# Kernel tuning notes

Hardware: AMD Instinct MI355X
Metric: run time of the kernel (lower is better)

## Reference

```python
import jax, jax.numpy as jnp
import numpy as np

B, S, H, NH, NKV, D = 1, 2048, 4096, 32, 8, 128
ROPE_BASE = 1000000.0


def setup_inputs() -> dict:
    key = jax.random.key(0)
    k0, k1, k2, k3, k4 = jax.random.split(key, 5)
    hidden_states = jax.random.normal(k0, (B, S, H), dtype=jnp.float32)
    Wq = jax.random.normal(k1, (NH * D, H), dtype=jnp.float32) * 0.02
    Wk = jax.random.normal(k2, (NKV * D, H), dtype=jnp.float32) * 0.02
    Wv = jax.random.normal(k3, (NKV * D, H), dtype=jnp.float32) * 0.02
    Wo = jax.random.normal(k4, (NH * D, NH * D), dtype=jnp.float32) * 0.02
    # RoPE tables (Mistral rope_theta = 1e6), concatenated-halves layout
    inv_freq = 1.0 / (ROPE_BASE ** (jnp.arange(0, D, 2, dtype=jnp.float32) / D))
    pos = jnp.arange(S, dtype=jnp.float32)
    freqs = pos[:, None] * inv_freq[None, :]            # [S, D/2]
    emb = jnp.concatenate([freqs, freqs], axis=-1)       # [S, D]
    cos = jnp.cos(emb)[None]                             # [1, S, D]
    sin = jnp.sin(emb)[None]
    # additive causal mask [1,1,S,S]
    causal = jnp.tril(jnp.ones((S, S), dtype=bool))
    attention_mask = jnp.where(causal, 0.0, -1e9).astype(jnp.float32)[None, None]
    return {"hidden_states": hidden_states, "cos": cos, "sin": sin,
            "attention_mask": attention_mask, "Wq": Wq, "Wk": Wk, "Wv": Wv, "Wo": Wo}


def _rotate_half(x):
    d = x.shape[-1] // 2
    return jnp.concatenate([-x[..., d:], x[..., :d]], axis=-1)


def reference(hidden_states, cos, sin, attention_mask, Wq, Wk, Wv, Wo):
    b, s, _ = hidden_states.shape
    nh = Wq.shape[0] // D
    nkv = Wk.shape[0] // D
    g = nh // nkv  # GQA groups
    scaling = D ** -0.5

    q = (hidden_states @ Wq.T).reshape(b, s, nh, D).transpose(0, 2, 1, 3)   # [b,nh,s,d]
    k = (hidden_states @ Wk.T).reshape(b, s, nkv, D).transpose(0, 2, 1, 3)  # [b,nkv,s,d]
    v = (hidden_states @ Wv.T).reshape(b, s, nkv, D).transpose(0, 2, 1, 3)

    c = cos[:, None]  # [b,1,s,d] broadcast over heads (unsqueeze_dim=1)
    sn = sin[:, None]
    q = q * c + _rotate_half(q) * sn
    k = k * c + _rotate_half(k) * sn

    # grouped-query attention without materializing repeated K/V
    qg = q.reshape(b, nkv, g, s, D)
    attn = jnp.einsum('bkgqd,bksd->bkgqs', qg, k) * scaling
    attn = attn + attention_mask[:, :, None]  # broadcast [1,1,1,s,s]
    w = jax.nn.softmax(attn.astype(jnp.float32), axis=-1).astype(q.dtype)
    out = jnp.einsum('bkgqs,bksd->bkgqd', w, v)  # [b,nkv,g,s,d]
    out = out.reshape(b, nh, s, D).transpose(0, 2, 1, 3).reshape(b, s, nh * D)
    return out @ Wo.T
```

## Files before the change

### kernel.cpp

```cpp
#include <hip/hip_runtime.h>
#include <hip/hip_bf16.h>
#include <cstdint>
#include <cstddef>

#define S_LEN 2048
#define HID   4096
#define NHEAD 32
#define NKVH  8
#define HD    128
#define QKV_STR 6144

typedef __bf16 bf16x8 __attribute__((ext_vector_type(8)));
typedef float  f32x4  __attribute__((ext_vector_type(4)));
typedef float  f32x16 __attribute__((ext_vector_type(16)));

__device__ __forceinline__ unsigned short f2bf(float f) {
  union { float f; unsigned int u; } c; c.f = f;
  unsigned int u = c.u;
  return (unsigned short)((u + 0x7fffu + ((u >> 16) & 1u)) >> 16);
}
__device__ __forceinline__ void gload16(const void* g, void* l) {
  __builtin_amdgcn_global_load_lds((const __attribute__((address_space(1))) void*)g,
                                   (__attribute__((address_space(3))) void*)l, 16, 0, 0);
}

__global__ void cvt_multi(const float* __restrict__ s0, const float* __restrict__ s1,
                          const float* __restrict__ s2, const float* __restrict__ s3,
                          const float* __restrict__ s4,
                          unsigned short* __restrict__ d0, unsigned short* __restrict__ d1,
                          unsigned short* __restrict__ d2, unsigned short* __restrict__ d3,
                          unsigned short* __restrict__ d4,
                          int n0, int n1, int n2, int n3, int n4c) {
  const float* src; unsigned short* dst; int n;
  switch (blockIdx.y) {
    case 0: src = s0; dst = d0; n = n0; break;
    case 1: src = s1; dst = d1; n = n1; break;
    case 2: src = s2; dst = d2; n = n2; break;
    case 3: src = s3; dst = d3; n = n3; break;
    default: src = s4; dst = d4; n = n4c; break;
  }
  int i = blockIdx.x * blockDim.x + threadIdx.x;
  int stride = gridDim.x * blockDim.x;
  for (; i < n; i += stride) {
    float4 v = ((const float4*)src)[i];
    ushort4 o;
    o.x = f2bf(v.x); o.y = f2bf(v.y); o.z = f2bf(v.z); o.w = f2bf(v.w);
    ((ushort4*)dst)[i] = o;
  }
}

template <bool F32OUT>
__global__ __launch_bounds__(256)
void gemm_bt(const unsigned short* __restrict__ A,
             const unsigned short* __restrict__ Bm,
             void* __restrict__ Cout, int N, int K) {
  __shared__ __align__(16) unsigned short lA[3][128 * 32];
  __shared__ __align__(16) unsigned short lB[3][128 * 32];
  const int tid = threadIdx.x;
  const int lane = tid & 63, wid = tid >> 6;
  const int l15 = lane & 15, lg = lane >> 4;
  const int wr = (wid >> 1) * 64, wc = (wid & 1) * 64;
  const int nwg = gridDim.x * 16;
  int bid = blockIdx.x + blockIdx.y * gridDim.x;
  bid = (bid & 7) * (nwg >> 3) + (bid >> 3);
  const int bm = bid & 15, bn = bid >> 4;

  f32x4 acc[4][4] = {};
  const unsigned short* Ab = A + (size_t)bm * 128 * K;
  const unsigned short* Bb = Bm + (size_t)bn * 128 * K;

  auto stage = [&](int t, int buf) {
    const int k0 = t * 32;
#pragma unroll
    for (int i = 0; i < 2; ++i) {
      int c = tid + i * 256;
      int row = c >> 2, sl = c & 3;
      int g = sl ^ ((row >> 1) & 3);
      gload16(Ab + (size_t)row * K + k0 + g * 8, (char*)lA[buf] + c * 16);
      gload16(Bb + (size_t)row * K + k0 + g * 8, (char*)lB[buf] + c * 16);
    }
  };

  const int nt = K / 32;
  stage(0, 0);
  if (nt > 1) stage(1, 1);
  const int swz = (l15 >> 1) & 3;

  int cur = 0;
  for (int t = 0; t < nt; ++t) {
    if (t + 1 < nt) asm volatile("s_waitcnt vmcnt(4)" ::: "memory");
    else            asm volatile("s_waitcnt vmcnt(0)" ::: "memory");
    __builtin_amdgcn_s_barrier();
    __builtin_amdgcn_sched_barrier(0);
    if (t + 2 < nt) { int nb = cur + 2; if (nb >= 3) nb -= 3; stage(t + 2, nb); }
    bf16x8 af[4], bfr[4];
#pragma unroll
    for (int m = 0; m < 4; ++m)
      af[m] = *(const bf16x8*)&lA[cur][(wr + m * 16 + l15) * 32 + ((lg ^ swz) * 8)];
#pragma unroll
    for (int n = 0; n < 4; ++n)
      bfr[n] = *(const bf16x8*)&lB[cur][(wc + n * 16 + l15) * 32 + ((lg ^ swz) * 8)];
#pragma unroll
    for (int m = 0; m < 4; ++m)
#pragma unroll
      for (int n = 0; n < 4; ++n)
        acc[m][n] = __builtin_amdgcn_mfma_f32_16x16x32_bf16(af[m], bfr[n], acc[m][n], 0, 0, 0);
    ++cur; if (cur >= 3) cur -= 3;
  }
  const int r0 = bm * 128 + wr + 4 * lg;
  const int c0 = bn * 128 + wc + l15;
#pragma unroll
  for (int m = 0; m < 4; ++m)
#pragma unroll
    for (int n = 0; n < 4; ++n)
#pragma unroll
      for (int j = 0; j < 4; ++j) {
        size_t idx = (size_t)(r0 + m * 16 + j) * N + (c0 + n * 16);
        if (F32OUT) ((float*)Cout)[idx] = acc[m][n][j];
        else        ((unsigned short*)Cout)[idx] = f2bf(acc[m][n][j]);
      }
}

__global__ void rope_kernel(unsigned short* __restrict__ X,
                            const float* __restrict__ cp,
                            const float* __restrict__ sp, int lognh, int rs) {
  int idx = blockIdx.x * blockDim.x + threadIdx.x;
  int d = idx & 63;
  int head = (idx >> 6) & ((1 << lognh) - 1);
  int s = idx >> (6 + lognh);
  float c = cp[s * 128 + d], sn = sp[s * 128 + d];
  size_t base = (size_t)s * rs + (head << 7) + d;
  float x1 = __bfloat162float(*(const __hip_bfloat16*)&X[base]);
  float x2 = __bfloat162float(*(const __hip_bfloat16*)&X[base + 64]);
  X[base]      = f2bf(x1 * c - x2 * sn);
  X[base + 64] = f2bf(x2 * c + x1 * sn);
}

__global__ __launch_bounds__(256)
void transpose_v(const unsigned short* __restrict__ qkv,
                 unsigned short* __restrict__ VT) {
  __shared__ __align__(16) unsigned short tile[128 * 128];
  const int tid = threadIdx.x;
  const int s0 = blockIdx.x * 128;
  const int kvh = blockIdx.y;
  const unsigned short* src = qkv + 5120 + kvh * 128;
#pragma unroll
  for (int i = 0; i < 8; ++i) {
    int c = tid + i * 256;
    int s = c >> 4, dc = c & 15;
    int f = (s ^ (s >> 3)) & 7;
    uint4 v = *(const uint4*)(src + (size_t)(s0 + s) * QKV_STR + dc * 8);
    *(uint4*)&tile[s * 128 + ((dc ^ f) * 8)] = v;
  }
  __syncthreads();
#pragma unroll
  for (int i = 0; i < 8; ++i) {
    int c = tid + i * 256;
    int d = c >> 4, sc = c & 15;
    unsigned short tmp[8];
#pragma unroll
    for (int j = 0; j < 8; ++j) {
      int s = sc * 8 + j;
      int f = (s ^ (s >> 3)) & 7;
      tmp[j] = tile[s * 128 + (((d >> 3) ^ f) * 8) + (d & 7)];
    }
    *(uint4*)(VT + ((size_t)kvh * 128 + d) * S_LEN + s0 + sc * 8) = *(uint4*)tmp;
  }
}

#define CROW(r) (((r) & 3) + 8 * ((r) >> 2) + 4 * hi)
__global__ __launch_bounds__(256, 2)
void flash_attn(const unsigned short* __restrict__ qkv,
                const unsigned short* __restrict__ VT,
                unsigned short* __restrict__ Og) {
  __shared__ __align__(16) unsigned short lK[2 * 64 * 128];
  __shared__ __align__(16) unsigned short lVt[2 * 128 * 64];
  const int tid = threadIdx.x;
  const int lane = tid & 63, w = tid >> 6;
  const int l31 = lane & 31, hi = lane >> 5;
  const int h = blockIdx.y, kvh = h >> 2;
  const int qt = (gridDim.x - 1) - blockIdx.x;
  const int nt = 2 * qt + 2;
  const int qlane = qt * 128 + w * 32 + l31;
  const int qmaxw = qt * 128 + w * 32 + 31;
  const float S2 = 0.12752960f;

  bf16x8 qf[8];
  {
    const unsigned short* qp = qkv + (size_t)qlane * QKV_STR + h * HD + hi * 8;
#pragma unroll
    for (int ks = 0; ks < 8; ++ks) qf[ks] = *(const bf16x8*)(qp + ks * 16);
  }
  f32x16 accO[4] = {};
  float m_run = -3e38f, l_run = 0.f;

  const unsigned short* Kb0 = qkv + 4096 + kvh * HD;
  const unsigned short* VTh = VT + (size_t)kvh * 128 * S_LEN;

  auto stageK = [&](int t, int buf) {
    const unsigned short* Kb = Kb0 + (size_t)(t * 64) * QKV_STR;
    char* dst = (char*)(lK + buf * (64 * 128));
#pragma unroll
    for (int i = 0; i < 4; ++i) {
      int c = tid + i * 256;
      int row = c >> 4, s = c & 15;
      gload16(Kb + (size_t)row * QKV_STR + ((s ^ (row & 7)) * 8), dst + c * 16);
    }
  };
  auto stageV = [&](int t, int buf) {
    const unsigned short* Vb = VTh + t * 64;
    char* dst = (char*)(lVt + buf * (128 * 64));
#pragma unroll
    for (int i = 0; i < 4; ++i) {
      int c = tid + i * 256;
      int d = c >> 3, s = c & 7;
      gload16(Vb + (size_t)d * S_LEN + ((s ^ (d & 7)) * 8), dst + c * 16);
    }
  };

  stageK(0, 0);
  stageV(0, 0);
  __syncthreads();

  int cur = 0;
  for (int t = 0; t < nt; ++t) {
    const bool pf = (t + 1 < nt);
    if (pf) { stageK(t + 1, cur ^ 1); stageV(t + 1, cur ^ 1); }

#pragma unroll
    for (int c2 = 0; c2 < 2; ++c2) {
      const int kvb = t * 64 + c2 * 32;
      if (kvb > qmaxw) continue;
      f32x16 st = {};
      const unsigned short* lKc = lK + cur * (64 * 128) + c2 * 32 * 128;
      __builtin_amdgcn_s_setprio(1);
#pragma unroll
      for (int ks = 0; ks < 8; ++ks) {
        bf16x8 kf = *(const bf16x8*)&lKc[l31 * 128 + (((ks * 2 + hi) ^ (l31 & 7)) * 8)];
        st = __builtin_amdgcn_mfma_f32_32x32x16_bf16(kf, qf[ks], st, 0, 0, 0);
      }
      __builtin_amdgcn_s_setprio(0);
      if (kvb + 31 > qt * 128 + w * 32) {
#pragma unroll
        for (int r = 0; r < 16; ++r)
          if (kvb + CROW(r) > qlane) st[r] = -3e38f;
      }
      float t0 = fmaxf(st[0], st[1]),  t1 = fmaxf(st[2], st[3]);
      float t2 = fmaxf(st[4], st[5]),  t3 = fmaxf(st[6], st[7]);
      float t4 = fmaxf(st[8], st[9]),  t5 = fmaxf(st[10], st[11]);
      float t6 = fmaxf(st[12], st[13]), t7 = fmaxf(st[14], st[15]);
      float tm = fmaxf(fmaxf(fmaxf(t0, t1), fmaxf(t2, t3)),
                       fmaxf(fmaxf(t4, t5), fmaxf(t6, t7)));
      tm = fmaxf(tm, __shfl_xor(tm, 32));
      const bool skip = __all(tm <= m_run);
      float corr = 1.f;
      if (!skip) {
        float mnew = fmaxf(m_run, tm);
        corr = __builtin_amdgcn_exp2f((m_run - mnew) * S2);
        m_run = mnew;
      }
      const float mS2 = m_run * S2;
      float p[16];
#pragma unroll
      for (int r = 0; r < 16; ++r) p[r] = __builtin_amdgcn_exp2f(st[r] * S2 - mS2);
      float s0b = (p[0] + p[1]) + (p[2] + p[3]);
      float s1b = (p[4] + p[5]) + (p[6] + p[7]);
      float s2b = (p[8] + p[9]) + (p[10] + p[11]);
      float s3b = (p[12] + p[13]) + (p[14] + p[15]);
      float rsum = (s0b + s1b) + (s2b + s3b);
      rsum += __shfl_xor(rsum, 32);
      l_run = l_run * corr + rsum;
      if (!skip) {
#pragma unroll
        for (int db = 0; db < 4; ++db) accO[db] = accO[db] * corr;
      }
      unsigned wpk[8], xpk[8];
#pragma unroll
      for (int i = 0; i < 8; ++i) {
        __hip_bfloat162 b2 = __float22bfloat162_rn(float2{p[2 * i], p[2 * i + 1]});
        wpk[i] = *(unsigned*)&b2;
        xpk[i] = (unsigned)__shfl_xor((int)wpk[i], 32);
      }
      int4 pa0i, pa1i;
      pa0i.x = hi ? (int)xpk[2] : (int)wpk[0]; pa0i.y = hi ? (int)xpk[3] : (int)wpk[1];
      pa0i.z = hi ? (int)wpk[2] : (int)xpk[0]; pa0i.w = hi ? (int)wpk[3] : (int)xpk[1];
      pa1i.x = hi ? (int)xpk[6] : (int)wpk[4]; pa1i.y = hi ? (int)xpk[7] : (int)wpk[5];
      pa1i.z = hi ? (int)wpk[6] : (int)xpk[4]; pa1i.w = hi ? (int)wpk[7] : (int)xpk[5];
      bf16x8 pa0 = *(bf16x8*)&pa0i, pa1 = *(bf16x8*)&pa1i;
      const unsigned short* lVc = lVt + cur * (128 * 64);
      __builtin_amdgcn_s_setprio(1);
#pragma unroll
      for (int db = 0; db < 4; ++db) {
        int d = db * 32 + l31;
#pragma unroll
        for (int ks2 = 0; ks2 < 2; ++ks2) {
          int ck = c2 * 4 + ks2 * 2 + hi;
          bf16x8 vf = *(const bf16x8*)&lVc[d * 64 + ((ck ^ (d & 7)) * 8)];
          accO[db] = __builtin_amdgcn_mfma_f32_32x32x16_bf16(vf, ks2 ? pa1 : pa0, accO[db], 0, 0, 0);
        }
      }
      __builtin_amdgcn_s_setprio(0);
    }
    __syncthreads();
    cur ^= 1;
  }

  const float invl = 1.0f / l_run;
  unsigned short* orow = Og + (size_t)(qt * 128 + w * 32 + l31) * HID + h * HD;
#pragma unroll
  for (int db = 0; db < 4; ++db)
#pragma unroll
    for (int rr = 0; rr < 4; ++rr) {
      int d0 = db * 32 + rr * 8 + 4 * hi;
      ushort4 o;
      o.x = f2bf(accO[db][rr * 4 + 0] * invl);
      o.y = f2bf(accO[db][rr * 4 + 1] * invl);
      o.z = f2bf(accO[db][rr * 4 + 2] * invl);
      o.w = f2bf(accO[db][rr * 4 + 3] * invl);
      *(ushort4*)(orow + d0) = o;
    }
}

extern "C" void kernel_launch(void* const* d_in, const int* in_sizes, int n_in,
                              void* d_out, int out_size, void* d_ws, size_t ws_size,
                              hipStream_t stream) {
  const float* hs   = (const float*)d_in[0];
  const float* cosp = (const float*)d_in[1];
  const float* sinp = (const float*)d_in[2];
  const float* Wq = (const float*)d_in[4];
  const float* Wk = (const float*)d_in[5];
  const float* Wv = (const float*)d_in[6];
  const float* Wo = (const float*)d_in[7];
  float* out = (float*)d_out;

  uint8_t* ws = (uint8_t*)d_ws;
  size_t off = 0;
  auto alloc = [&](size_t bytes) { void* p = ws + off; off += bytes; return p; };
  unsigned short* hidB  = (unsigned short*)alloc((size_t)S_LEN * HID * 2);
  unsigned short* wqkvB = (unsigned short*)alloc((size_t)QKV_STR * HID * 2);
  unsigned short* woB   = (unsigned short*)alloc((size_t)HID * HID * 2);
  unsigned short* qkvB  = (unsigned short*)alloc((size_t)S_LEN * QKV_STR * 2);
  unsigned short* aoB   = (unsigned short*)alloc((size_t)S_LEN * HID * 2);
  unsigned short* vtB   = (unsigned short*)alloc((size_t)NKVH * HD * S_LEN * 2);

  cvt_multi<<<dim3(1024, 5), 256, 0, stream>>>(
      hs, Wq, Wk, Wv, Wo,
      hidB, wqkvB, wqkvB + (size_t)HID * HID, wqkvB + (size_t)(HID + 1024) * HID, woB,
      S_LEN * HID / 4, HID * HID / 4, 1024 * HID / 4, 1024 * HID / 4, HID * HID / 4);

  gemm_bt<false><<<dim3(QKV_STR / 128, S_LEN / 128), 256, 0, stream>>>(
      hidB, wqkvB, qkvB, QKV_STR, HID);

  rope_kernel<<<(S_LEN * NHEAD * 64) / 256, 256, 0, stream>>>(qkvB, cosp, sinp, 5, QKV_STR);
  rope_kernel<<<(S_LEN * NKVH * 64) / 256, 256, 0, stream>>>(qkvB + HID, cosp, sinp, 3, QKV_STR);

  transpose_v<<<dim3(S_LEN / 128, NKVH), 256, 0, stream>>>(qkvB, vtB);

  flash_attn<<<dim3(S_LEN / 128, NHEAD), 256, 0, stream>>>(qkvB, vtB, aoB);

  gemm_bt<true><<<dim3(HID / 128, S_LEN / 128), 256, 0, stream>>>(
      aoB, woB, out, HID, HID);
}
```

Measured before the change: 367.4 us.

## Templatize GEMM tile shape, add lazy softmax rescale and permlane32 swap

```diff
diff --git a/kernel.cpp b/kernel.cpp
--- a/kernel.cpp
+++ b/kernel.cpp
@@ -13,6 +13,7 @@
 typedef __bf16 bf16x8 __attribute__((ext_vector_type(8)));
 typedef float  f32x4  __attribute__((ext_vector_type(4)));
 typedef float  f32x16 __attribute__((ext_vector_type(16)));
+typedef unsigned uint32x2_t __attribute__((ext_vector_type(2)));
 
 __device__ __forceinline__ unsigned short f2bf(float f) {
   union { float f; unsigned int u; } c; c.f = f;
@@ -49,34 +50,42 @@
   }
 }
 
-template <bool F32OUT>
-__global__ __launch_bounds__(256)
+template <int MR, int NR, bool F32OUT>
+__global__ __launch_bounds__(256, 2)
 void gemm_bt(const unsigned short* __restrict__ A,
              const unsigned short* __restrict__ Bm,
              void* __restrict__ Cout, int N, int K) {
-  __shared__ __align__(16) unsigned short lA[3][128 * 32];
-  __shared__ __align__(16) unsigned short lB[3][128 * 32];
+  constexpr int BM = 32 * MR, BN = 32 * NR;
+  constexpr int BLKM = 2048 / BM;
+  __shared__ __align__(16) unsigned short lA[3][BM * 32];
+  __shared__ __align__(16) unsigned short lB[3][BN * 32];
   const int tid = threadIdx.x;
   const int lane = tid & 63, wid = tid >> 6;
   const int l15 = lane & 15, lg = lane >> 4;
-  const int wr = (wid >> 1) * 64, wc = (wid & 1) * 64;
-  const int nwg = gridDim.x * 16;
+  const int wr = (wid >> 1) * (BM / 2), wc = (wid & 1) * (BN / 2);
+  const int nwg = gridDim.x * gridDim.y;
   int bid = blockIdx.x + blockIdx.y * gridDim.x;
   bid = (bid & 7) * (nwg >> 3) + (bid >> 3);
-  const int bm = bid & 15, bn = bid >> 4;
-
-  f32x4 acc[4][4] = {};
-  const unsigned short* Ab = A + (size_t)bm * 128 * K;
-  const unsigned short* Bb = Bm + (size_t)bn * 128 * K;
+  const int bm = bid % BLKM, bn = bid / BLKM;
+
+  f32x4 acc[MR][NR] = {};
+  const unsigned short* Ab = A + (size_t)bm * BM * K;
+  const unsigned short* Bb = Bm + (size_t)bn * BN * K;
 
   auto stage = [&](int t, int buf) {
     const int k0 = t * 32;
 #pragma unroll
-    for (int i = 0; i < 2; ++i) {
+    for (int i = 0; i < BM / 64; ++i) {
       int c = tid + i * 256;
       int row = c >> 2, sl = c & 3;
       int g = sl ^ ((row >> 1) & 3);
       gload16(Ab + (size_t)row * K + k0 + g * 8, (char*)lA[buf] + c * 16);
+    }
+#pragma unroll
+    for (int i = 0; i < BN / 64; ++i) {
+      int c = tid + i * 256;
+      int row = c >> 2, sl = c & 3;
+      int g = sl ^ ((row >> 1) & 3);
       gload16(Bb + (size_t)row * K + k0 + g * 8, (char*)lB[buf] + c * 16);
     }
   };
@@ -88,31 +97,35 @@
 
   int cur = 0;
   for (int t = 0; t < nt; ++t) {
-    if (t + 1 < nt) asm volatile("s_waitcnt vmcnt(4)" ::: "memory");
-    else            asm volatile("s_waitcnt vmcnt(0)" ::: "memory");
+    if (t + 1 < nt) {
+      if constexpr ((BM + BN) / 64 == 4) asm volatile("s_waitcnt vmcnt(4)" ::: "memory");
+      else                               asm volatile("s_waitcnt vmcnt(6)" ::: "memory");
+    } else {
+      asm volatile("s_waitcnt vmcnt(0)" ::: "memory");
+    }
     __builtin_amdgcn_s_barrier();
     __builtin_amdgcn_sched_barrier(0);
     if (t + 2 < nt) { int nb = cur + 2; if (nb >= 3) nb -= 3; stage(t + 2, nb); }
-    bf16x8 af[4], bfr[4];
-#pragma unroll
-    for (int m = 0; m < 4; ++m)
+    bf16x8 af[MR], bfr[NR];
+#pragma unroll
+    for (int m = 0; m < MR; ++m)
       af[m] = *(const bf16x8*)&lA[cur][(wr + m * 16 + l15) * 32 + ((lg ^ swz) * 8)];
 #pragma unroll
-    for (int n = 0; n < 4; ++n)
+    for (int n = 0; n < NR; ++n)
       bfr[n] = *(const bf16x8*)&lB[cur][(wc + n * 16 + l15) * 32 + ((lg ^ swz) * 8)];
 #pragma unroll
-    for (int m = 0; m < 4; ++m)
-#pragma unroll
-      for (int n = 0; n < 4; ++n)
+    for (int m = 0; m < MR; ++m)
+#pragma unroll
+      for (int n = 0; n < NR; ++n)
         acc[m][n] = __builtin_amdgcn_mfma_f32_16x16x32_bf16(af[m], bfr[n], acc[m][n], 0, 0, 0);
     ++cur; if (cur >= 3) cur -= 3;
   }
-  const int r0 = bm * 128 + wr + 4 * lg;
-  const int c0 = bn * 128 + wc + l15;
-#pragma unroll
-  for (int m = 0; m < 4; ++m)
-#pragma unroll
-    for (int n = 0; n < 4; ++n)
+  const int r0 = bm * BM + wr + 4 * lg;
+  const int c0 = bn * BN + wc + l15;
+#pragma unroll
+  for (int m = 0; m < MR; ++m)
+#pragma unroll
+    for (int n = 0; n < NR; ++n)
 #pragma unroll
       for (int j = 0; j < 4; ++j) {
         size_t idx = (size_t)(r0 + m * 16 + j) * N + (c0 + n * 16);
@@ -252,7 +265,7 @@
       float tm = fmaxf(fmaxf(fmaxf(t0, t1), fmaxf(t2, t3)),
                        fmaxf(fmaxf(t4, t5), fmaxf(t6, t7)));
       tm = fmaxf(tm, __shfl_xor(tm, 32));
-      const bool skip = __all(tm <= m_run);
+      const bool skip = __all((tm - m_run) * S2 <= 8.0f);
       float corr = 1.f;
       if (!skip) {
         float mnew = fmaxf(m_run, tm);
@@ -274,18 +287,29 @@
 #pragma unroll
         for (int db = 0; db < 4; ++db) accO[db] = accO[db] * corr;
       }
-      unsigned wpk[8], xpk[8];
+      unsigned wpk[8];
 #pragma unroll
       for (int i = 0; i < 8; ++i) {
         __hip_bfloat162 b2 = __float22bfloat162_rn(float2{p[2 * i], p[2 * i + 1]});
         wpk[i] = *(unsigned*)&b2;
-        xpk[i] = (unsigned)__shfl_xor((int)wpk[i], 32);
       }
       int4 pa0i, pa1i;
+#if __has_builtin(__builtin_amdgcn_permlane32_swap)
+      uint32x2_t r0 = __builtin_amdgcn_permlane32_swap(wpk[0], wpk[2], false, false);
+      uint32x2_t r1 = __builtin_amdgcn_permlane32_swap(wpk[1], wpk[3], false, false);
+      uint32x2_t r2 = __builtin_amdgcn_permlane32_swap(wpk[4], wpk[6], false, false);
+      uint32x2_t r3 = __builtin_amdgcn_permlane32_swap(wpk[5], wpk[7], false, false);
+      pa0i.x = (int)r0.x; pa0i.y = (int)r1.x; pa0i.z = (int)r0.y; pa0i.w = (int)r1.y;
+      pa1i.x = (int)r2.x; pa1i.y = (int)r3.x; pa1i.z = (int)r2.y; pa1i.w = (int)r3.y;
+#else
+      unsigned xpk[8];
+#pragma unroll
+      for (int i = 0; i < 8; ++i) xpk[i] = (unsigned)__shfl_xor((int)wpk[i], 32);
       pa0i.x = hi ? (int)xpk[2] : (int)wpk[0]; pa0i.y = hi ? (int)xpk[3] : (int)wpk[1];
       pa0i.z = hi ? (int)wpk[2] : (int)xpk[0]; pa0i.w = hi ? (int)wpk[3] : (int)xpk[1];
       pa1i.x = hi ? (int)xpk[6] : (int)wpk[4]; pa1i.y = hi ? (int)xpk[7] : (int)wpk[5];
       pa1i.z = hi ? (int)wpk[6] : (int)xpk[4]; pa1i.w = hi ? (int)wpk[7] : (int)xpk[5];
+#endif
       bf16x8 pa0 = *(bf16x8*)&pa0i, pa1 = *(bf16x8*)&pa1i;
       const unsigned short* lVc = lVt + cur * (128 * 64);
       __builtin_amdgcn_s_setprio(1);
@@ -348,7 +372,7 @@
       hidB, wqkvB, wqkvB + (size_t)HID * HID, wqkvB + (size_t)(HID + 1024) * HID, woB,
       S_LEN * HID / 4, HID * HID / 4, 1024 * HID / 4, 1024 * HID / 4, HID * HID / 4);
 
-  gemm_bt<false><<<dim3(QKV_STR / 128, S_LEN / 128), 256, 0, stream>>>(
+  gemm_bt<8, 4, false><<<dim3(QKV_STR / 128, S_LEN / 256), 256, 0, stream>>>(
       hidB, wqkvB, qkvB, QKV_STR, HID);
 
   rope_kernel<<<(S_LEN * NHEAD * 64) / 256, 256, 0, stream>>>(qkvB, cosp, sinp, 5, QKV_STR);
@@ -358,6 +382,6 @@
 
   flash_attn<<<dim3(S_LEN / 128, NHEAD), 256, 0, stream>>>(qkvB, vtB, aoB);
 
-  gemm_bt<true><<<dim3(HID / 128, S_LEN / 128), 256, 0, stream>>>(
+  gemm_bt<4, 4, true><<<dim3(HID / 128, S_LEN / 128), 256, 0, stream>>>(
       aoB, woB, out, HID, HID);
 }
```

Result: slower. 376.8 us (+2.5%).

## Use 8-wave 128x256 GEMM tiles, lazy softmax rescale, and permlane32 swap

Applied to the files above, without the earlier changes.

```diff
diff --git a/kernel.cpp b/kernel.cpp
--- a/kernel.cpp
+++ b/kernel.cpp
@@ -13,6 +13,7 @@
 typedef __bf16 bf16x8 __attribute__((ext_vector_type(8)));
 typedef float  f32x4  __attribute__((ext_vector_type(4)));
 typedef float  f32x16 __attribute__((ext_vector_type(16)));
+typedef unsigned uint32x2_t __attribute__((ext_vector_type(2)));
 
 __device__ __forceinline__ unsigned short f2bf(float f) {
   union { float f; unsigned int u; } c; c.f = f;
@@ -50,65 +51,136 @@
 }
 
 template <bool F32OUT>
-__global__ __launch_bounds__(256)
-void gemm_bt(const unsigned short* __restrict__ A,
-             const unsigned short* __restrict__ Bm,
-             void* __restrict__ Cout, int N, int K) {
-  __shared__ __align__(16) unsigned short lA[3][128 * 32];
-  __shared__ __align__(16) unsigned short lB[3][128 * 32];
+__global__ __launch_bounds__(512, 1)
+void gemm8p(const unsigned short* __restrict__ A,
+            const unsigned short* __restrict__ Bm,
+            void* __restrict__ Cout, int N, int K) {
+  __shared__ __align__(16) unsigned short lA[3][128 * 64];
+  __shared__ __align__(16) unsigned short lB[3][256 * 64];
   const int tid = threadIdx.x;
   const int lane = tid & 63, wid = tid >> 6;
   const int l15 = lane & 15, lg = lane >> 4;
-  const int wr = (wid >> 1) * 64, wc = (wid & 1) * 64;
-  const int nwg = gridDim.x * 16;
+  const int wm = wid >> 2, wn = wid & 3;
+  const int wr = wm * 64, wc = wn * 64;
+  const int nwg = gridDim.x * gridDim.y;
   int bid = blockIdx.x + blockIdx.y * gridDim.x;
   bid = (bid & 7) * (nwg >> 3) + (bid >> 3);
   const int bm = bid & 15, bn = bid >> 4;
 
   f32x4 acc[4][4] = {};
   const unsigned short* Ab = A + (size_t)bm * 128 * K;
-  const unsigned short* Bb = Bm + (size_t)bn * 128 * K;
-
-  auto stage = [&](int t, int buf) {
-    const int k0 = t * 32;
+  const unsigned short* Bb = Bm + (size_t)bn * 256 * K;
+
+  auto stageA = [&](int t, int buf) {
+    const int k0 = t * 64;
 #pragma unroll
     for (int i = 0; i < 2; ++i) {
-      int c = tid + i * 256;
-      int row = c >> 2, sl = c & 3;
-      int g = sl ^ ((row >> 1) & 3);
+      int c = tid + i * 512;
+      int row = c >> 3, ch = c & 7;
+      int g = ch ^ (row & 7);
       gload16(Ab + (size_t)row * K + k0 + g * 8, (char*)lA[buf] + c * 16);
+    }
+  };
+  auto stageB = [&](int t, int buf, int half) {
+    const int k0 = t * 64;
+#pragma unroll
+    for (int i = 0; i < 2; ++i) {
+      int c = tid + (half * 2 + i) * 512;
+      int row = c >> 3, ch = c & 7;
+      int g = ch ^ (row & 7);
       gload16(Bb + (size_t)row * K + k0 + g * 8, (char*)lB[buf] + c * 16);
     }
   };
-
-  const int nt = K / 32;
-  stage(0, 0);
-  if (nt > 1) stage(1, 1);
-  const int swz = (l15 >> 1) & 3;
+  auto rdA = [&](int buf, int m, int ks) -> bf16x8 {
+    int row = wr + m * 16 + l15;
+    int ch = (ks * 4 + lg) ^ (row & 7);
+    return *(const bf16x8*)&lA[buf][row * 64 + ch * 8];
+  };
+  auto rdB = [&](int buf, int n, int ks) -> bf16x8 {
+    int row = wc + n * 16 + l15;
+    int ch = (ks * 4 + lg) ^ (row & 7);
+    return *(const bf16x8*)&lB[buf][row * 64 + ch * 8];
+  };
+
+  const int nt = K / 64;
+  stageA(0, 0); stageB(0, 0, 0); stageB(0, 0, 1);
+  stageA(1, 1); stageB(1, 1, 0); stageB(1, 1, 1);
 
   int cur = 0;
   for (int t = 0; t < nt; ++t) {
-    if (t + 1 < nt) asm volatile("s_waitcnt vmcnt(4)" ::: "memory");
+    if (t + 1 < nt) asm volatile("s_waitcnt vmcnt(6)" ::: "memory");
     else            asm volatile("s_waitcnt vmcnt(0)" ::: "memory");
     __builtin_amdgcn_s_barrier();
     __builtin_amdgcn_sched_barrier(0);
-    if (t + 2 < nt) { int nb = cur + 2; if (nb >= 3) nb -= 3; stage(t + 2, nb); }
-    bf16x8 af[4], bfr[4];
-#pragma unroll
-    for (int m = 0; m < 4; ++m)
-      af[m] = *(const bf16x8*)&lA[cur][(wr + m * 16 + l15) * 32 + ((lg ^ swz) * 8)];
-#pragma unroll
-    for (int n = 0; n < 4; ++n)
-      bfr[n] = *(const bf16x8*)&lB[cur][(wc + n * 16 + l15) * 32 + ((lg ^ swz) * 8)];
-#pragma unroll
-    for (int m = 0; m < 4; ++m)
-#pragma unroll
-      for (int n = 0; n < 4; ++n)
-        acc[m][n] = __builtin_amdgcn_mfma_f32_16x16x32_bf16(af[m], bfr[n], acc[m][n], 0, 0, 0);
+    int nb = cur + 2; if (nb >= 3) nb -= 3;
+    const bool pf = (t + 2 < nt);
+    bf16x8 b0, b1, b2, b3, a0, a1;
+
+    if (pf) stageA(t + 2, nb);
+    a0 = rdA(cur, 0, 0); a1 = rdA(cur, 1, 0);
+    b0 = rdB(cur, 0, 0); b1 = rdB(cur, 1, 0);
+    b2 = rdB(cur, 2, 0); b3 = rdB(cur, 3, 0);
+    __builtin_amdgcn_s_setprio(1);
+    acc[0][0] = __builtin_amdgcn_mfma_f32_16x16x32_bf16(a0, b0, acc[0][0], 0, 0, 0);
+    acc[0][1] = __builtin_amdgcn_mfma_f32_16x16x32_bf16(a0, b1, acc[0][1], 0, 0, 0);
+    acc[0][2] = __builtin_amdgcn_mfma_f32_16x16x32_bf16(a0, b2, acc[0][2], 0, 0, 0);
+    acc[0][3] = __builtin_amdgcn_mfma_f32_16x16x32_bf16(a0, b3, acc[0][3], 0, 0, 0);
+    acc[1][0] = __builtin_amdgcn_mfma_f32_16x16x32_bf16(a1, b0, acc[1][0], 0, 0, 0);
+    acc[1][1] = __builtin_amdgcn_mfma_f32_16x16x32_bf16(a1, b1, acc[1][1], 0, 0, 0);
+    acc[1][2] = __builtin_amdgcn_mfma_f32_16x16x32_bf16(a1, b2, acc[1][2], 0, 0, 0);
+    acc[1][3] = __builtin_amdgcn_mfma_f32_16x16x32_bf16(a1, b3, acc[1][3], 0, 0, 0);
+    __builtin_amdgcn_s_setprio(0);
+    __builtin_amdgcn_s_barrier();
+    __builtin_amdgcn_sched_barrier(0);
+
+    if (pf) stageB(t + 2, nb, 0);
+    a0 = rdA(cur, 2, 0); a1 = rdA(cur, 3, 0);
+    __builtin_amdgcn_s_setprio(1);
+    acc[2][0] = __builtin_amdgcn_mfma_f32_16x16x32_bf16(a0, b0, acc[2][0], 0, 0, 0);
+    acc[2][1] = __builtin_amdgcn_mfma_f32_16x16x32_bf16(a0, b1, acc[2][1], 0, 0, 0);
+    acc[2][2] = __builtin_amdgcn_mfma_f32_16x16x32_bf16(a0, b2, acc[2][2], 0, 0, 0);
+    acc[2][3] = __builtin_amdgcn_mfma_f32_16x16x32_bf16(a0, b3, acc[2][3], 0, 0, 0);
+    acc[3][0] = __builtin_amdgcn_mfma_f32_16x16x32_bf16(a1, b0, acc[3][0], 0, 0, 0);
+    acc[3][1] = __builtin_amdgcn_mfma_f32_16x16x32_bf16(a1, b1, acc[3][1], 0, 0, 0);
+    acc[3][2] = __builtin_amdgcn_mfma_f32_16x16x32_bf16(a1, b2, acc[3][2], 0, 0, 0);
+    acc[3][3] = __builtin_amdgcn_mfma_f32_16x16x32_bf16(a1, b3, acc[3][3], 0, 0, 0);
+    __builtin_amdgcn_s_setprio(0);
+    __builtin_amdgcn_s_barrier();
+    __builtin_amdgcn_sched_barrier(0);
+
+    if (pf) stageB(t + 2, nb, 1);
+    a0 = rdA(cur, 0, 1); a1 = rdA(cur, 1, 1);
+    b0 = rdB(cur, 0, 1); b1 = rdB(cur, 1, 1);
+    b2 = rdB(cur, 2, 1); b3 = rdB(cur, 3, 1);
+    __builtin_amdgcn_s_setprio(1);
+    acc[0][0] = __builtin_amdgcn_mfma_f32_16x16x32_bf16(a0, b0, acc[0][0], 0, 0, 0);
+    acc[0][1] = __builtin_amdgcn_mfma_f32_16x16x32_bf16(a0, b1, acc[0][1], 0, 0, 0);
+    acc[0][2] = __builtin_amdgcn_mfma_f32_16x16x32_bf16(a0, b2, acc[0][2], 0, 0, 0);
+    acc[0][3] = __builtin_amdgcn_mfma_f32_16x16x32_bf16(a0, b3, acc[0][3], 0, 0, 0);
+    acc[1][0] = __builtin_amdgcn_mfma_f32_16x16x32_bf16(a1, b0, acc[1][0], 0, 0, 0);
+    acc[1][1] = __builtin_amdgcn_mfma_f32_16x16x32_bf16(a1, b1, acc[1][1], 0, 0, 0);
+    acc[1][2] = __builtin_amdgcn_mfma_f32_16x16x32_bf16(a1, b2, acc[1][2], 0, 0, 0);
+    acc[1][3] = __builtin_amdgcn_mfma_f32_16x16x32_bf16(a1, b3, acc[1][3], 0, 0, 0);
+    __builtin_amdgcn_s_setprio(0);
+    __builtin_amdgcn_s_barrier();
+    __builtin_amdgcn_sched_barrier(0);
+
+    a0 = rdA(cur, 2, 1); a1 = rdA(cur, 3, 1);
+    __builtin_amdgcn_s_setprio(1);
+    acc[2][0] = __builtin_amdgcn_mfma_f32_16x16x32_bf16(a0, b0, acc[2][0], 0, 0, 0);
+    acc[2][1] = __builtin_amdgcn_mfma_f32_16x16x32_bf16(a0, b1, acc[2][1], 0, 0, 0);
+    acc[2][2] = __builtin_amdgcn_mfma_f32_16x16x32_bf16(a0, b2, acc[2][2], 0, 0, 0);
+    acc[2][3] = __builtin_amdgcn_mfma_f32_16x16x32_bf16(a0, b3, acc[2][3], 0, 0, 0);
+    acc[3][0] = __builtin_amdgcn_mfma_f32_16x16x32_bf16(a1, b0, acc[3][0], 0, 0, 0);
+    acc[3][1] = __builtin_amdgcn_mfma_f32_16x16x32_bf16(a1, b1, acc[3][1], 0, 0, 0);
+    acc[3][2] = __builtin_amdgcn_mfma_f32_16x16x32_bf16(a1, b2, acc[3][2], 0, 0, 0);
+    acc[3][3] = __builtin_amdgcn_mfma_f32_16x16x32_bf16(a1, b3, acc[3][3], 0, 0, 0);
+    __builtin_amdgcn_s_setprio(0);
     ++cur; if (cur >= 3) cur -= 3;
   }
+
   const int r0 = bm * 128 + wr + 4 * lg;
-  const int c0 = bn * 128 + wc + l15;
+  const int c0 = bn * 256 + wc + l15;
 #pragma unroll
   for (int m = 0; m < 4; ++m)
 #pragma unroll
@@ -252,7 +324,7 @@
       float tm = fmaxf(fmaxf(fmaxf(t0, t1), fmaxf(t2, t3)),
                        fmaxf(fmaxf(t4, t5), fmaxf(t6, t7)));
       tm = fmaxf(tm, __shfl_xor(tm, 32));
-      const bool skip = __all(tm <= m_run);
+      const bool skip = __all((tm - m_run) * S2 <= 8.0f);
       float corr = 1.f;
       if (!skip) {
         float mnew = fmaxf(m_run, tm);
@@ -274,18 +346,29 @@
 #pragma unroll
         for (int db = 0; db < 4; ++db) accO[db] = accO[db] * corr;
       }
-      unsigned wpk[8], xpk[8];
+      unsigned wpk[8];
 #pragma unroll
       for (int i = 0; i < 8; ++i) {
         __hip_bfloat162 b2 = __float22bfloat162_rn(float2{p[2 * i], p[2 * i + 1]});
         wpk[i] = *(unsigned*)&b2;
-        xpk[i] = (unsigned)__shfl_xor((int)wpk[i], 32);
       }
       int4 pa0i, pa1i;
+#if __has_builtin(__builtin_amdgcn_permlane32_swap)
+      uint32x2_t r0 = __builtin_amdgcn_permlane32_swap(wpk[0], wpk[2], false, false);
+      uint32x2_t r1 = __builtin_amdgcn_permlane32_swap(wpk[1], wpk[3], false, false);
+      uint32x2_t r2 = __builtin_amdgcn_permlane32_swap(wpk[4], wpk[6], false, false);
+      uint32x2_t r3 = __builtin_amdgcn_permlane32_swap(wpk[5], wpk[7], false, false);
+      pa0i.x = (int)r0.x; pa0i.y = (int)r1.x; pa0i.z = (int)r0.y; pa0i.w = (int)r1.y;
+      pa1i.x = (int)r2.x; pa1i.y = (int)r3.x; pa1i.z = (int)r2.y; pa1i.w = (int)r3.y;
+#else
+      unsigned xpk[8];
+#pragma unroll
+      for (int i = 0; i < 8; ++i) xpk[i] = (unsigned)__shfl_xor((int)wpk[i], 32);
       pa0i.x = hi ? (int)xpk[2] : (int)wpk[0]; pa0i.y = hi ? (int)xpk[3] : (int)wpk[1];
       pa0i.z = hi ? (int)wpk[2] : (int)xpk[0]; pa0i.w = hi ? (int)wpk[3] : (int)xpk[1];
       pa1i.x = hi ? (int)xpk[6] : (int)wpk[4]; pa1i.y = hi ? (int)xpk[7] : (int)wpk[5];
       pa1i.z = hi ? (int)wpk[6] : (int)xpk[4]; pa1i.w = hi ? (int)wpk[7] : (int)xpk[5];
+#endif
       bf16x8 pa0 = *(bf16x8*)&pa0i, pa1 = *(bf16x8*)&pa1i;
       const unsigned short* lVc = lVt + cur * (128 * 64);
       __builtin_amdgcn_s_setprio(1);
@@ -348,7 +431,7 @@
       hidB, wqkvB, wqkvB + (size_t)HID * HID, wqkvB + (size_t)(HID + 1024) * HID, woB,
       S_LEN * HID / 4, HID * HID / 4, 1024 * HID / 4, 1024 * HID / 4, HID * HID / 4);
 
-  gemm_bt<false><<<dim3(QKV_STR / 128, S_LEN / 128), 256, 0, stream>>>(
+  gemm8p<false><<<dim3(QKV_STR / 256, S_LEN / 128), 512, 0, stream>>>(
       hidB, wqkvB, qkvB, QKV_STR, HID);
 
   rope_kernel<<<(S_LEN * NHEAD * 64) / 256, 256, 0, stream>>>(qkvB, cosp, sinp, 5, QKV_STR);
@@ -358,6 +441,6 @@
 
   flash_attn<<<dim3(S_LEN / 128, NHEAD), 256, 0, stream>>>(qkvB, vtB, aoB);
 
-  gemm_bt<true><<<dim3(HID / 128, S_LEN / 128), 256, 0, stream>>>(
+  gemm8p<true><<<dim3(HID / 256, S_LEN / 128), 512, 0, stream>>>(
       aoB, woB, out, HID, HID);
 }
```

New measurement: 484.2 us. 31.8% more time.

## Fuse Q RoPE into attention, lazy max rescale, permlane32 swap for P

Applied to the files above, without the earlier changes.

```diff
diff --git a/kernel.cpp b/kernel.cpp
--- a/kernel.cpp
+++ b/kernel.cpp
@@ -13,11 +13,16 @@
 typedef __bf16 bf16x8 __attribute__((ext_vector_type(8)));
 typedef float  f32x4  __attribute__((ext_vector_type(4)));
 typedef float  f32x16 __attribute__((ext_vector_type(16)));
+typedef unsigned uint32x2_t __attribute__((ext_vector_type(2)));
 
 __device__ __forceinline__ unsigned short f2bf(float f) {
   union { float f; unsigned int u; } c; c.f = f;
   unsigned int u = c.u;
   return (unsigned short)((u + 0x7fffu + ((u >> 16) & 1u)) >> 16);
+}
+__device__ __forceinline__ float bf2f(unsigned short b) {
+  union { unsigned int u; float f; } c; c.u = ((unsigned int)b) << 16;
+  return c.f;
 }
 __device__ __forceinline__ void gload16(const void* g, void* l) {
   __builtin_amdgcn_global_load_lds((const __attribute__((address_space(1))) void*)g,
@@ -130,8 +135,8 @@
   int s = idx >> (6 + lognh);
   float c = cp[s * 128 + d], sn = sp[s * 128 + d];
   size_t base = (size_t)s * rs + (head << 7) + d;
-  float x1 = __bfloat162float(*(const __hip_bfloat16*)&X[base]);
-  float x2 = __bfloat162float(*(const __hip_bfloat16*)&X[base + 64]);
+  float x1 = bf2f(X[base]);
+  float x2 = bf2f(X[base + 64]);
   X[base]      = f2bf(x1 * c - x2 * sn);
   X[base + 64] = f2bf(x2 * c + x1 * sn);
 }
@@ -172,6 +177,8 @@
 __global__ __launch_bounds__(256, 2)
 void flash_attn(const unsigned short* __restrict__ qkv,
                 const unsigned short* __restrict__ VT,
+                const float* __restrict__ cp,
+                const float* __restrict__ sp,
                 unsigned short* __restrict__ Og) {
   __shared__ __align__(16) unsigned short lK[2 * 64 * 128];
   __shared__ __align__(16) unsigned short lVt[2 * 128 * 64];
@@ -190,6 +197,23 @@
     const unsigned short* qp = qkv + (size_t)qlane * QKV_STR + h * HD + hi * 8;
 #pragma unroll
     for (int ks = 0; ks < 8; ++ks) qf[ks] = *(const bf16x8*)(qp + ks * 16);
+    const float* crow = cp + (size_t)qlane * 128 + hi * 8;
+    const float* srow = sp + (size_t)qlane * 128 + hi * 8;
+#pragma unroll
+    for (int ks = 0; ks < 4; ++ks) {
+      float4 c0 = *(const float4*)(crow + ks * 16);
+      float4 c1 = *(const float4*)(crow + ks * 16 + 4);
+      float4 s0 = *(const float4*)(srow + ks * 16);
+      float4 s1 = *(const float4*)(srow + ks * 16 + 4);
+      float cc[8] = {c0.x, c0.y, c0.z, c0.w, c1.x, c1.y, c1.z, c1.w};
+      float ss[8] = {s0.x, s0.y, s0.z, s0.w, s1.x, s1.y, s1.z, s1.w};
+#pragma unroll
+      for (int j = 0; j < 8; ++j) {
+        float x1 = (float)qf[ks][j], x2 = (float)qf[ks + 4][j];
+        qf[ks][j]     = (__bf16)(x1 * cc[j] - x2 * ss[j]);
+        qf[ks + 4][j] = (__bf16)(x2 * cc[j] + x1 * ss[j]);
+      }
+    }
   }
   f32x16 accO[4] = {};
   float m_run = -3e38f, l_run = 0.f;
@@ -252,7 +276,7 @@
       float tm = fmaxf(fmaxf(fmaxf(t0, t1), fmaxf(t2, t3)),
                        fmaxf(fmaxf(t4, t5), fmaxf(t6, t7)));
       tm = fmaxf(tm, __shfl_xor(tm, 32));
-      const bool skip = __all(tm <= m_run);
+      const bool skip = __all((tm - m_run) * S2 <= 8.0f);
       float corr = 1.f;
       if (!skip) {
         float mnew = fmaxf(m_run, tm);
@@ -274,18 +298,29 @@
 #pragma unroll
         for (int db = 0; db < 4; ++db) accO[db] = accO[db] * corr;
       }
-      unsigned wpk[8], xpk[8];
+      unsigned wpk[8];
 #pragma unroll
       for (int i = 0; i < 8; ++i) {
         __hip_bfloat162 b2 = __float22bfloat162_rn(float2{p[2 * i], p[2 * i + 1]});
         wpk[i] = *(unsigned*)&b2;
-        xpk[i] = (unsigned)__shfl_xor((int)wpk[i], 32);
       }
       int4 pa0i, pa1i;
+#if __has_builtin(__builtin_amdgcn_permlane32_swap)
+      uint32x2_t r0 = __builtin_amdgcn_permlane32_swap(wpk[0], wpk[2], false, false);
+      uint32x2_t r1 = __builtin_amdgcn_permlane32_swap(wpk[1], wpk[3], false, false);
+      uint32x2_t r2 = __builtin_amdgcn_permlane32_swap(wpk[4], wpk[6], false, false);
+      uint32x2_t r3 = __builtin_amdgcn_permlane32_swap(wpk[5], wpk[7], false, false);
+      pa0i.x = (int)r0.x; pa0i.y = (int)r1.x; pa0i.z = (int)r0.y; pa0i.w = (int)r1.y;
+      pa1i.x = (int)r2.x; pa1i.y = (int)r3.x; pa1i.z = (int)r2.y; pa1i.w = (int)r3.y;
+#else
+      unsigned xpk[8];
+#pragma unroll
+      for (int i = 0; i < 8; ++i) xpk[i] = (unsigned)__shfl_xor((int)wpk[i], 32);
       pa0i.x = hi ? (int)xpk[2] : (int)wpk[0]; pa0i.y = hi ? (int)xpk[3] : (int)wpk[1];
       pa0i.z = hi ? (int)wpk[2] : (int)xpk[0]; pa0i.w = hi ? (int)wpk[3] : (int)xpk[1];
       pa1i.x = hi ? (int)xpk[6] : (int)wpk[4]; pa1i.y = hi ? (int)xpk[7] : (int)wpk[5];
       pa1i.z = hi ? (int)wpk[6] : (int)xpk[4]; pa1i.w = hi ? (int)wpk[7] : (int)xpk[5];
+#endif
       bf16x8 pa0 = *(bf16x8*)&pa0i, pa1 = *(bf16x8*)&pa1i;
       const unsigned short* lVc = lVt + cur * (128 * 64);
       __builtin_amdgcn_s_setprio(1);
@@ -351,12 +386,11 @@
   gemm_bt<false><<<dim3(QKV_STR / 128, S_LEN / 128), 256, 0, stream>>>(
       hidB, wqkvB, qkvB, QKV_STR, HID);
 
-  rope_kernel<<<(S_LEN * NHEAD * 64) / 256, 256, 0, stream>>>(qkvB, cosp, sinp, 5, QKV_STR);
   rope_kernel<<<(S_LEN * NKVH * 64) / 256, 256, 0, stream>>>(qkvB + HID, cosp, sinp, 3, QKV_STR);
 
   transpose_v<<<dim3(S_LEN / 128, NKVH), 256, 0, stream>>>(qkvB, vtB);
 
-  flash_attn<<<dim3(S_LEN / 128, NHEAD), 256, 0, stream>>>(qkvB, vtB, aoB);
+  flash_attn<<<dim3(S_LEN / 128, NHEAD), 256, 0, stream>>>(qkvB, vtB, cosp, sinp, aoB);
 
   gemm_bt<true><<<dim3(HID / 128, S_LEN / 128), 256, 0, stream>>>(
       aoB, woB, out, HID, HID);
```

After: 349.9 us. 1.05x faster.
